# Optimization experiments

Hardware: AMD Instinct MI355X
Metric: run time of the kernel (lower is better)

## Reference

```python
import jax, jax.numpy as jnp
import numpy as np

B, S, D = 46, 50, 768
GAMA = 1.0 - 2.0 ** -5  # 1 - np.power(2.0, -5 - arange(0,1)) -> scalar 0.96875


def make_pe(n, d):
    # PositionalEncoding buffer pe[:n]; note original adds pe[:emb.size(0)],
    # i.e. the encoding is indexed by BATCH position (faithful to source).
    position = jnp.arange(n, dtype=jnp.float32)[:, None]
    div_term = jnp.exp(jnp.arange(0, d, 2, dtype=jnp.float32) * (-np.log(10000.0) / d))
    pe = jnp.zeros((n, d), dtype=jnp.float32)
    pe = pe.at[:, 0::2].set(jnp.sin(position * div_term))
    pe = pe.at[:, 1::2].set(jnp.cos(position * div_term))
    return pe[:, None, :]  # [n, 1, d] broadcasts over the seq dim


def setup_inputs() -> dict:
    key = jax.random.key(0)
    ks = jax.random.split(key, 6)
    w = lambda k, shape: jax.random.normal(k, shape, dtype=jnp.float32) * 0.02
    return {
        "text_embedding": jax.random.normal(ks[0], (B, S, D), dtype=jnp.float32),
        "embedding": jax.random.normal(ks[1], (B, S, D), dtype=jnp.float32),
        "Wq_w": w(ks[2], (D, D)), "Wq_b": jnp.zeros((D,), jnp.float32),
        "Wk_w": w(ks[3], (D, D)), "Wk_b": jnp.zeros((D,), jnp.float32),
        "Wv_w": w(ks[4], (D, D)), "Wv_b": jnp.zeros((D,), jnp.float32),
        "lin_w": w(ks[5], (S, D)), "lin_b": jnp.zeros((S,), jnp.float32),
    }


def reference(text_embedding, embedding, Wq_w, Wq_b, Wk_w, Wk_b, Wv_w, Wv_b, lin_w, lin_b):
    b = text_embedding.shape[0]
    pe = make_pe(b, D)  # [B,1,D]
    # dropout p=0.1 is identity in eval mode
    Q = text_embedding @ Wq_w.T + Wq_b + pe          # [B,S,D]
    K = embedding @ Wk_w.T + Wk_b + pe               # [B,S,D]
    V = embedding @ Wv_w.T + Wv_b                    # [B,S,D]
    # head_num == 1, so transpose_for_scores is a no-op view
    Q_trans = Q @ lin_w.T + lin_b                    # [B,S,S] (S == 50)
    scores = jnp.einsum('bqd,bkd->bqk', Q, K) * 8.0  # scaling *8 as in source
    probs = jax.nn.softmax(scores, axis=-1)
    ctx = jnp.einsum('bqk,bkd->bqd', probs, V)       # [B,S,D] context_layer

    # RetNet-like gamma-decay recurrence over the batch dim (host-sync loop in
    # the original, expressed here as an on-device lax.scan):
    #   s_i = Q_trans @ (gama * s_{i-1}) + ctx[i],  s_{-1} = 0
    def step(s, c_i):  # s: [B,S,D], c_i: [S,D]
        s_new = jnp.einsum('bij,bjd->bid', Q_trans, GAMA * s) + c_i[None]
        return s_new, s_new
    _, rec = jax.lax.scan(step, jnp.zeros_like(ctx), ctx)  # [B,B,S,D]
    return ctx, rec
```

## Files before the change

kernel.cpp:

```cpp
#include <hip/hip_runtime.h>
#include <math.h>

#define NB 46
#define NS 50
#define ND 768
#define GAMA 0.96875f
#define NM 2300

using bfrag  = __attribute__((ext_vector_type(8))) short;
using f32x16 = __attribute__((ext_vector_type(16))) float;

union FragU { unsigned u[4]; bfrag f; };

__device__ __forceinline__ void cvt_hilo(const float f[8], bfrag& fh, bfrag& fl)
{
    FragU uh, ul;
    #pragma unroll
    for (int t = 0; t < 4; t++) {
        const unsigned b0 = __float_as_uint(f[2 * t]);
        const unsigned b1 = __float_as_uint(f[2 * t + 1]);
        uh.u[t] = (b0 >> 16) | (b1 & 0xFFFF0000u);
        const float r0 = f[2 * t]     - __uint_as_float(b0 & 0xFFFF0000u);
        const float r1 = f[2 * t + 1] - __uint_as_float(b1 & 0xFFFF0000u);
        ul.u[t] = (__float_as_uint(r0) >> 16) | (__float_as_uint(r1) & 0xFFFF0000u);
    }
    fh = uh.f; fl = ul.f;
}

__global__ __launch_bounds__(256) void qkv_gemm(
    const float* __restrict__ text_emb, const float* __restrict__ emb,
    const float* __restrict__ Wq, const float* __restrict__ bq,
    const float* __restrict__ Wk, const float* __restrict__ bk,
    const float* __restrict__ Wv, const float* __restrict__ bv,
    float* __restrict__ Q, float* __restrict__ K, float* __restrict__ V)
{
    const int z = blockIdx.z;
    const float* X    = (z == 0) ? text_emb : emb;
    const float* W    = (z == 0) ? Wq : (z == 1) ? Wk : Wv;
    const float* bias = (z == 0) ? bq : (z == 1) ? bk : bv;
    float* out        = (z == 0) ? Q  : (z == 1) ? K  : V;

    __shared__ float Xs[32][68];
    __shared__ float Ws[32][68];

    const int tid = threadIdx.x;
    const int w   = tid >> 6;
    const int l   = tid & 63;
    const int c   = l & 31;
    const int h   = l >> 5;
    const int wm  = w >> 1, wn = w & 1;
    const int m0  = blockIdx.x * 64, n0 = blockIdx.y * 64;

    const int lrow = tid >> 2;
    const int lk   = (tid & 3) * 4;
    const int xm   = m0 + lrow;
    const float* __restrict__ Xrow = X + (size_t)(xm < NM ? xm : 0) * ND;
    const float* __restrict__ Wrow = W + (size_t)(n0 + lrow) * ND;

    f32x16 acc;
    #pragma unroll
    for (int g = 0; g < 16; g++) acc[g] = 0.f;

    for (int k0 = 0; k0 < ND; k0 += 32) {
        const float4 xv0 = *reinterpret_cast<const float4*>(&Xrow[k0 + lk]);
        const float4 xv1 = *reinterpret_cast<const float4*>(&Xrow[k0 + 16 + lk]);
        const float4 wv0 = *reinterpret_cast<const float4*>(&Wrow[k0 + lk]);
        const float4 wv1 = *reinterpret_cast<const float4*>(&Wrow[k0 + 16 + lk]);
        __syncthreads();
        Xs[lk + 0][lrow] = xv0.x; Xs[lk + 1][lrow] = xv0.y;
        Xs[lk + 2][lrow] = xv0.z; Xs[lk + 3][lrow] = xv0.w;
        Xs[16 + lk + 0][lrow] = xv1.x; Xs[16 + lk + 1][lrow] = xv1.y;
        Xs[16 + lk + 2][lrow] = xv1.z; Xs[16 + lk + 3][lrow] = xv1.w;
        Ws[lk + 0][lrow] = wv0.x; Ws[lk + 1][lrow] = wv0.y;
        Ws[lk + 2][lrow] = wv0.z; Ws[lk + 3][lrow] = wv0.w;
        Ws[16 + lk + 0][lrow] = wv1.x; Ws[16 + lk + 1][lrow] = wv1.y;
        Ws[16 + lk + 2][lrow] = wv1.z; Ws[16 + lk + 3][lrow] = wv1.w;
        __syncthreads();

        #pragma unroll
        for (int kt = 0; kt < 2; kt++) {
            float fx[8], fw[8];
            #pragma unroll
            for (int j = 0; j < 8; j++) {
                fx[j] = Xs[16 * kt + 8 * h + j][32 * wm + c];
                fw[j] = Ws[16 * kt + 8 * h + j][32 * wn + c];
            }
            bfrag Ah, Al, Bh, Bl;
            cvt_hilo(fx, Ah, Al);
            cvt_hilo(fw, Bh, Bl);
            acc = __builtin_amdgcn_mfma_f32_32x32x16_bf16(Ah, Bh, acc, 0, 0, 0);
            acc = __builtin_amdgcn_mfma_f32_32x32x16_bf16(Ah, Bl, acc, 0, 0, 0);
            acc = __builtin_amdgcn_mfma_f32_32x32x16_bf16(Al, Bh, acc, 0, 0, 0);
        }
    }

    const float C2 = -0.0239861701969175f;
    const int n = n0 + 32 * wn + c;
    #pragma unroll
    for (int g = 0; g < 16; g++) {
        const int rr = (g & 3) + 8 * (g >> 2) + 4 * h;
        const int m  = m0 + 32 * wm + rr;
        if (m >= NM) continue;
        float v = acc[g] + bias[n];
        if (z < 2) {
            const int bpos = m / NS;
            const float ang = (float)bpos * expf((float)(n >> 1) * C2);
            v += (n & 1) ? cosf(ang) : sinf(ang);
        }
        out[(size_t)m * ND + n] = v;
    }
}

__global__ __launch_bounds__(256, 1) void attn(
    const float* __restrict__ Q, const float* __restrict__ K,
    const float* __restrict__ V,
    const float* __restrict__ lin_w, const float* __restrict__ lin_b,
    float* __restrict__ Ag, float* __restrict__ ctx_out)
{
    const int b   = blockIdx.x;
    const int tid = threadIdx.x;
    const int w   = tid >> 6;
    const int l   = tid & 63;
    const int c   = l & 31;
    const int h   = l >> 5;

    __shared__ float Lsh[9 * 64 * 68];
    float* SP = Lsh;
    float* QP = Lsh + 4 * 64 * 68;
    float* Pf = Lsh + 8 * 64 * 68;

    const float* __restrict__ Qb = Q + (size_t)b * NS * ND;
    const float* __restrict__ Kb = K + (size_t)b * NS * ND;
    const float* __restrict__ Vb = V + (size_t)b * NS * ND;

    f32x16 accS[2][2], accQ[2][2];
    #pragma unroll
    for (int mt = 0; mt < 2; mt++)
        #pragma unroll
        for (int nt = 0; nt < 2; nt++)
            #pragma unroll
            for (int g = 0; g < 16; g++) { accS[mt][nt][g] = 0.f; accQ[mt][nt][g] = 0.f; }

    const int ks = w * 192;
    for (int kt = 0; kt < 12; ++kt) {
        const int ko = ks + kt * 16 + 8 * h;
        bfrag Qh[2], Ql[2], Kh[2], Kl[2], Wh[2], Wl[2];
        #pragma unroll
        for (int mt = 0; mt < 2; mt++) {
            const int row = 32 * mt + c;
            const int r = (row < NS) ? row : 0;
            float f[8];
            {
                const float4 a0 = *reinterpret_cast<const float4*>(&Qb[(size_t)r * ND + ko]);
                const float4 a1 = *reinterpret_cast<const float4*>(&Qb[(size_t)r * ND + ko + 4]);
                f[0]=a0.x; f[1]=a0.y; f[2]=a0.z; f[3]=a0.w; f[4]=a1.x; f[5]=a1.y; f[6]=a1.z; f[7]=a1.w;
            }
            cvt_hilo(f, Qh[mt], Ql[mt]);
            {
                const float4 a0 = *reinterpret_cast<const float4*>(&Kb[(size_t)r * ND + ko]);
                const float4 a1 = *reinterpret_cast<const float4*>(&Kb[(size_t)r * ND + ko + 4]);
                f[0]=a0.x; f[1]=a0.y; f[2]=a0.z; f[3]=a0.w; f[4]=a1.x; f[5]=a1.y; f[6]=a1.z; f[7]=a1.w;
            }
            cvt_hilo(f, Kh[mt], Kl[mt]);
            {
                const float4 a0 = *reinterpret_cast<const float4*>(&lin_w[(size_t)r * ND + ko]);
                const float4 a1 = *reinterpret_cast<const float4*>(&lin_w[(size_t)r * ND + ko + 4]);
                f[0]=a0.x; f[1]=a0.y; f[2]=a0.z; f[3]=a0.w; f[4]=a1.x; f[5]=a1.y; f[6]=a1.z; f[7]=a1.w;
            }
            cvt_hilo(f, Wh[mt], Wl[mt]);
        }
        #pragma unroll
        for (int mt = 0; mt < 2; mt++)
            #pragma unroll
            for (int nt = 0; nt < 2; nt++) {
                f32x16 a = accS[mt][nt];
                a = __builtin_amdgcn_mfma_f32_32x32x16_bf16(Qh[mt], Kh[nt], a, 0, 0, 0);
                a = __builtin_amdgcn_mfma_f32_32x32x16_bf16(Qh[mt], Kl[nt], a, 0, 0, 0);
                a = __builtin_amdgcn_mfma_f32_32x32x16_bf16(Ql[mt], Kh[nt], a, 0, 0, 0);
                accS[mt][nt] = a;
                f32x16 q = accQ[mt][nt];
                q = __builtin_amdgcn_mfma_f32_32x32x16_bf16(Qh[mt], Wh[nt], q, 0, 0, 0);
                q = __builtin_amdgcn_mfma_f32_32x32x16_bf16(Qh[mt], Wl[nt], q, 0, 0, 0);
                q = __builtin_amdgcn_mfma_f32_32x32x16_bf16(Ql[mt], Wh[nt], q, 0, 0, 0);
                accQ[mt][nt] = q;
            }
    }

    {
        float* SPw = SP + w * (64 * 68);
        float* QPw = QP + w * (64 * 68);
        #pragma unroll
        for (int mt = 0; mt < 2; mt++)
            #pragma unroll
            for (int nt = 0; nt < 2; nt++)
                #pragma unroll
                for (int g = 0; g < 16; g++) {
                    const int rg  = 32 * mt + (g & 3) + 8 * (g >> 2) + 4 * h;
                    const int col = 32 * nt + c;
                    SPw[rg * 68 + col] = accS[mt][nt][g];
                    QPw[rg * 68 + col] = accQ[mt][nt][g];
                }
    }
    __syncthreads();

    {
        const int r  = tid >> 2;
        const int cg = (tid & 3) * 16;
        #pragma unroll
        for (int q4 = 0; q4 < 4; ++q4) {
            const int off = r * 68 + cg + q4 * 4;
            float4 s0 = *reinterpret_cast<const float4*>(&SP[off]);
            float4 s1 = *reinterpret_cast<const float4*>(&SP[64 * 68 + off]);
            float4 s2 = *reinterpret_cast<const float4*>(&SP[2 * 64 * 68 + off]);
            float4 s3 = *reinterpret_cast<const float4*>(&SP[3 * 64 * 68 + off]);
            float4 r4;
            r4.x = 8.f * ((s0.x + s1.x) + (s2.x + s3.x));
            r4.y = 8.f * ((s0.y + s1.y) + (s2.y + s3.y));
            r4.z = 8.f * ((s0.z + s1.z) + (s2.z + s3.z));
            r4.w = 8.f * ((s0.w + s1.w) + (s2.w + s3.w));
            *reinterpret_cast<float4*>(&SP[off]) = r4;
            float4 t0 = *reinterpret_cast<const float4*>(&QP[off]);
            float4 t1 = *reinterpret_cast<const float4*>(&QP[64 * 68 + off]);
            float4 t2 = *reinterpret_cast<const float4*>(&QP[2 * 64 * 68 + off]);
            float4 t3 = *reinterpret_cast<const float4*>(&QP[3 * 64 * 68 + off]);
            float4 u4;
            u4.x = (t0.x + t1.x) + (t2.x + t3.x);
            u4.y = (t0.y + t1.y) + (t2.y + t3.y);
            u4.z = (t0.z + t1.z) + (t2.z + t3.z);
            u4.w = (t0.w + t1.w) + (t2.w + t3.w);
            *reinterpret_cast<float4*>(&QP[off]) = u4;
        }
    }
    __syncthreads();

    if (tid < NS) {
        const float* Sr = SP + tid * 68;
        float mx = -INFINITY;
        for (int c2 = 0; c2 < NS; ++c2) mx = fmaxf(mx, Sr[c2]);
        float sum = 0.f;
        for (int c2 = 0; c2 < NS; ++c2) {
            const float e = expf(Sr[c2] - mx);
            Pf[tid * 68 + c2] = e;
            sum += e;
        }
        const float inv = 1.f / sum;
        for (int c2 = 0; c2 < NS; ++c2) Pf[tid * 68 + c2] *= inv;
        for (int c2 = NS; c2 < 64; ++c2) Pf[tid * 68 + c2] = 0.f;
    }
    for (int e = tid; e < NS * NS; e += 256) {
        const int r = e / NS, cc = e - r * NS;
        Ag[b * (NS * NS) + e] = GAMA * (QP[r * 68 + cc] + lin_b[cc]);
    }
    __syncthreads();

    bfrag Ph[2][4], Pl[2][4];
    #pragma unroll
    for (int mt = 0; mt < 2; mt++)
        #pragma unroll
        for (int kt = 0; kt < 4; kt++) {
            float f[8];
            #pragma unroll
            for (int j = 0; j < 8; j++)
                f[j] = Pf[(32 * mt + c) * 68 + kt * 16 + 8 * h + j];
            cvt_hilo(f, Ph[mt][kt], Pl[mt][kt]);
        }

    for (int j3 = 0; j3 < 3; ++j3) {
        const int dbase = (w * 3 + j3) * 64;
        f32x16 accC[2][2];
        #pragma unroll
        for (int mt = 0; mt < 2; mt++)
            #pragma unroll
            for (int nt = 0; nt < 2; nt++)
                #pragma unroll
                for (int g = 0; g < 16; g++) accC[mt][nt][g] = 0.f;

        #pragma unroll
        for (int nt = 0; nt < 2; nt++) {
            const int d = dbase + 32 * nt + c;
            #pragma unroll
            for (int kt = 0; kt < 4; kt++) {
                float f[8];
                #pragma unroll
                for (int j = 0; j < 8; j++) {
                    const int k2 = kt * 16 + 8 * h + j;
                    f[j] = (k2 < NS) ? Vb[(size_t)k2 * ND + d] : 0.f;
                }
                bfrag Bh, Bl;
                cvt_hilo(f, Bh, Bl);
                #pragma unroll
                for (int mt = 0; mt < 2; mt++) {
                    f32x16 a = accC[mt][nt];
                    a = __builtin_amdgcn_mfma_f32_32x32x16_bf16(Ph[mt][kt], Bh, a, 0, 0, 0);
                    a = __builtin_amdgcn_mfma_f32_32x32x16_bf16(Ph[mt][kt], Bl, a, 0, 0, 0);
                    a = __builtin_amdgcn_mfma_f32_32x32x16_bf16(Pl[mt][kt], Bh, a, 0, 0, 0);
                    accC[mt][nt] = a;
                }
            }
        }
        #pragma unroll
        for (int mt = 0; mt < 2; mt++)
            #pragma unroll
            for (int nt = 0; nt < 2; nt++)
                #pragma unroll
                for (int g = 0; g < 16; g++) {
                    const int rg = 32 * mt + (g & 3) + 8 * (g >> 2) + 4 * h;
                    if (rg < NS)
                        ctx_out[((size_t)b * NS + rg) * ND + dbase + 32 * nt + c] = accC[mt][nt][g];
                }
    }
}

__device__ __forceinline__ void rec2_step(
    int i, int b, int d0, int c, int h, int wid, int srow, int scol,
    const bfrag (&Ah)[4], const bfrag (&Al)[4],
    float4 (&creg)[4],
    const float* SfR, float* SfW, float* Cx,
    const float* __restrict__ ctx, float* __restrict__ rec)
{
    #pragma unroll
    for (int it = 0; it < 4; ++it) {
        const int r = (4 * wid + it) * 8 + srow;
        if (r < NS)
            *reinterpret_cast<float4*>(&Cx[r * 32 + scol]) = creg[it];
    }
    if (i + 1 < NB) {
        const float* __restrict__ src = ctx + (size_t)(i + 1) * NS * ND + d0;
        #pragma unroll
        for (int it = 0; it < 4; ++it) {
            const int r = (4 * wid + it) * 8 + srow;
            if (r < NS)
                creg[it] = *reinterpret_cast<const float4*>(&src[(size_t)r * ND + scol]);
        }
    }
    f32x16 acc;
    #pragma unroll
    for (int g = 0; g < 16; g++) {
        const int rg = 32 * wid + (g & 3) + 8 * (g >> 2) + 4 * h;
        acc[g] = Cx[rg * 32 + c];
    }
    #pragma unroll
    for (int kt = 0; kt < 4; kt++) {
        float f[8];
        #pragma unroll
        for (int j = 0; j < 8; j++)
            f[j] = SfR[(16 * kt + 8 * h + j) * 32 + c];
        bfrag Bh, Bl;
        cvt_hilo(f, Bh, Bl);
        acc = __builtin_amdgcn_mfma_f32_32x32x16_bf16(Ah[kt], Bh, acc, 0, 0, 0);
        acc = __builtin_amdgcn_mfma_f32_32x32x16_bf16(Ah[kt], Bl, acc, 0, 0, 0);
        acc = __builtin_amdgcn_mfma_f32_32x32x16_bf16(Al[kt], Bh, acc, 0, 0, 0);
    }
    #pragma unroll
    for (int g = 0; g < 16; g++) {
        const int rg = 32 * wid + (g & 3) + 8 * (g >> 2) + 4 * h;
        SfW[rg * 32 + c] = acc[g];
    }
    float* __restrict__ reci = rec + (size_t)(i * NB + b) * NS * ND + d0;
    #pragma unroll
    for (int it = 0; it < 4; ++it) {
        const int r = (4 * wid + it) * 8 + srow;
        if (r < NS) {
            const float4 v = *reinterpret_cast<const float4*>(&SfW[r * 32 + scol]);
            *reinterpret_cast<float4*>(&reci[(size_t)r * ND + scol]) = v;
        }
    }
    asm volatile("s_waitcnt lgkmcnt(0)" ::: "memory");
    __builtin_amdgcn_s_barrier();
    asm volatile("" ::: "memory");
}

__global__ __launch_bounds__(128, 2) void recur(
    const float* __restrict__ Ag, const float* __restrict__ ctx,
    float* __restrict__ rec)
{
    const int blk   = blockIdx.x;
    const int b     = blk / 24;
    const int chunk = blk - b * 24;
    const int tid   = threadIdx.x;
    const int wid   = tid >> 6;
    const int l     = tid & 63;
    const int c     = l & 31;
    const int h     = l >> 5;
    const int d0    = chunk * 32;
    const int srow  = l >> 3;
    const int scol  = (l & 7) * 4;

    __shared__ float Sfa[64 * 32];
    __shared__ float Sfb[64 * 32];
    __shared__ float Cx [64 * 32];

    const float* __restrict__ Ab = Ag + b * (NS * NS);
    bfrag Ah[4], Al[4];
    {
        const int row = 32 * wid + c;
        const bool rok = row < NS;
        const float* __restrict__ Arow = Ab + row * NS;
        #pragma unroll
        for (int kt = 0; kt < 4; kt++) {
            FragU uh, ul;
            #pragma unroll
            for (int t = 0; t < 4; t++) {
                const int k0 = 16 * kt + 8 * h + 2 * t;
                const float e = (rok && k0     < NS) ? Arow[k0]     : 0.f;
                const float o = (rok && k0 + 1 < NS) ? Arow[k0 + 1] : 0.f;
                const unsigned ue = __float_as_uint(e), uo = __float_as_uint(o);
                uh.u[t] = (ue >> 16) | (uo & 0xFFFF0000u);
                const float re = e - __uint_as_float(ue & 0xFFFF0000u);
                const float ro = o - __uint_as_float(uo & 0xFFFF0000u);
                ul.u[t] = (__float_as_uint(re) >> 16) | (__float_as_uint(ro) & 0xFFFF0000u);
            }
            Ah[kt] = uh.f; Al[kt] = ul.f;
        }
    }

    for (int idx = tid; idx < 14 * 32; idx += 128) {
        const int rr = 50 + (idx >> 5), cc = idx & 31;
        Cx [rr * 32 + cc] = 0.f;
        Sfa[rr * 32 + cc] = 0.f;
    }

    float4 creg[4];
    #pragma unroll
    for (int it = 0; it < 4; ++it) creg[it] = make_float4(0.f, 0.f, 0.f, 0.f);
    {
        const float* __restrict__ src = ctx + d0;
        float4 c0[4];
        #pragma unroll
        for (int it = 0; it < 4; ++it) {
            c0[it] = make_float4(0.f, 0.f, 0.f, 0.f);
            const int r = (4 * wid + it) * 8 + srow;
            if (r < NS)
                c0[it] = *reinterpret_cast<const float4*>(&src[(size_t)r * ND + scol]);
        }
        const float* __restrict__ s1 = ctx + (size_t)NS * ND + d0;
        #pragma unroll
        for (int it = 0; it < 4; ++it) {
            const int r = (4 * wid + it) * 8 + srow;
            if (r < NS)
                creg[it] = *reinterpret_cast<const float4*>(&s1[(size_t)r * ND + scol]);
        }
        float* __restrict__ r0 = rec + (size_t)b * NS * ND + d0;
        #pragma unroll
        for (int it = 0; it < 4; ++it) {
            const int r = (4 * wid + it) * 8 + srow;
            if (r < NS) {
                *reinterpret_cast<float4*>(&Sfa[r * 32 + scol]) = c0[it];
                *reinterpret_cast<float4*>(&r0[(size_t)r * ND + scol]) = c0[it];
            }
        }
    }
    asm volatile("s_waitcnt lgkmcnt(0)" ::: "memory");
    __builtin_amdgcn_s_barrier();
    asm volatile("" ::: "memory");

    int i = 1;
    for (; i + 1 < NB; i += 2) {
        rec2_step(i,     b, d0, c, h, wid, srow, scol, Ah, Al, creg, Sfa, Sfb, Cx, ctx, rec);
        rec2_step(i + 1, b, d0, c, h, wid, srow, scol, Ah, Al, creg, Sfb, Sfa, Cx, ctx, rec);
    }
    if (i < NB)
        rec2_step(i, b, d0, c, h, wid, srow, scol, Ah, Al, creg, Sfa, Sfb, Cx, ctx, rec);
}

extern "C" void kernel_launch(void* const* d_in, const int* in_sizes, int n_in,
                              void* d_out, int out_size, void* d_ws, size_t ws_size,
                              hipStream_t stream) {
    const float* text_emb = (const float*)d_in[0];
    const float* emb      = (const float*)d_in[1];
    const float* Wq = (const float*)d_in[2]; const float* bq = (const float*)d_in[3];
    const float* Wk = (const float*)d_in[4]; const float* bk = (const float*)d_in[5];
    const float* Wv = (const float*)d_in[6]; const float* bv = (const float*)d_in[7];
    const float* lw = (const float*)d_in[8]; const float* lb = (const float*)d_in[9];

    float* out = (float*)d_out;
    float* ctx = out;
    float* rec = out + NB * NS * ND;

    float* ws = (float*)d_ws;
    float* Q  = ws;
    float* K  = Q + NB * NS * ND;
    float* V  = K + NB * NS * ND;
    float* Ag = V + NB * NS * ND;

    qkv_gemm<<<dim3(36, 12, 3), 256, 0, stream>>>(text_emb, emb, Wq, bq, Wk, bk, Wv, bv, Q, K, V);
    attn<<<dim3(NB), 256, 0, stream>>>(Q, K, V, lw, lb, Ag, ctx);
    recur<<<dim3(1104), 128, 0, stream>>>(Ag, ctx, rec);
}
```

Before: 206.0 us.

## Restructure recurrence kernel to single-wave blocks with 16x16 MFMA tiles

The recurrence kernel now runs one 64-thread wave per block over a 16-column slice (2208 blocks), using 16x16x32 bf16 MFMA with four M-tiles instead of two waves with 32x32x16 tiles. Because a single wave owns the whole 64-row state tile, the per-step workgroup barrier and double-buffered shared state are removed and a single in-place buffer is used. This aims to remove the barrier latency on the serial 45-step chain and raise parallelism, at the cost of more blocks, narrower 64-byte global row segments, and more MFMA issues per step per wave.

```diff
diff --git a/kernel.cpp b/kernel.cpp
--- a/kernel.cpp
+++ b/kernel.cpp
@@ -9,6 +9,7 @@
 
 using bfrag  = __attribute__((ext_vector_type(8))) short;
 using f32x16 = __attribute__((ext_vector_type(16))) float;
+using f32x4  = __attribute__((ext_vector_type(4)))  float;
 
 union FragU { unsigned u[4]; bfrag f; };
 
@@ -311,97 +312,36 @@
     }
 }
 
-__device__ __forceinline__ void rec2_step(
-    int i, int b, int d0, int c, int h, int wid, int srow, int scol,
-    const bfrag (&Ah)[4], const bfrag (&Al)[4],
-    float4 (&creg)[4],
-    const float* SfR, float* SfW, float* Cx,
-    const float* __restrict__ ctx, float* __restrict__ rec)
-{
-    #pragma unroll
-    for (int it = 0; it < 4; ++it) {
-        const int r = (4 * wid + it) * 8 + srow;
-        if (r < NS)
-            *reinterpret_cast<float4*>(&Cx[r * 32 + scol]) = creg[it];
-    }
-    if (i + 1 < NB) {
-        const float* __restrict__ src = ctx + (size_t)(i + 1) * NS * ND + d0;
-        #pragma unroll
-        for (int it = 0; it < 4; ++it) {
-            const int r = (4 * wid + it) * 8 + srow;
-            if (r < NS)
-                creg[it] = *reinterpret_cast<const float4*>(&src[(size_t)r * ND + scol]);
-        }
-    }
-    f32x16 acc;
-    #pragma unroll
-    for (int g = 0; g < 16; g++) {
-        const int rg = 32 * wid + (g & 3) + 8 * (g >> 2) + 4 * h;
-        acc[g] = Cx[rg * 32 + c];
-    }
-    #pragma unroll
-    for (int kt = 0; kt < 4; kt++) {
-        float f[8];
-        #pragma unroll
-        for (int j = 0; j < 8; j++)
-            f[j] = SfR[(16 * kt + 8 * h + j) * 32 + c];
-        bfrag Bh, Bl;
-        cvt_hilo(f, Bh, Bl);
-        acc = __builtin_amdgcn_mfma_f32_32x32x16_bf16(Ah[kt], Bh, acc, 0, 0, 0);
-        acc = __builtin_amdgcn_mfma_f32_32x32x16_bf16(Ah[kt], Bl, acc, 0, 0, 0);
-        acc = __builtin_amdgcn_mfma_f32_32x32x16_bf16(Al[kt], Bh, acc, 0, 0, 0);
-    }
-    #pragma unroll
-    for (int g = 0; g < 16; g++) {
-        const int rg = 32 * wid + (g & 3) + 8 * (g >> 2) + 4 * h;
-        SfW[rg * 32 + c] = acc[g];
-    }
-    float* __restrict__ reci = rec + (size_t)(i * NB + b) * NS * ND + d0;
-    #pragma unroll
-    for (int it = 0; it < 4; ++it) {
-        const int r = (4 * wid + it) * 8 + srow;
-        if (r < NS) {
-            const float4 v = *reinterpret_cast<const float4*>(&SfW[r * 32 + scol]);
-            *reinterpret_cast<float4*>(&reci[(size_t)r * ND + scol]) = v;
-        }
-    }
-    asm volatile("s_waitcnt lgkmcnt(0)" ::: "memory");
-    __builtin_amdgcn_s_barrier();
-    asm volatile("" ::: "memory");
-}
-
-__global__ __launch_bounds__(128, 2) void recur(
+__global__ __launch_bounds__(64, 1) void recur(
     const float* __restrict__ Ag, const float* __restrict__ ctx,
     float* __restrict__ rec)
 {
     const int blk   = blockIdx.x;
-    const int b     = blk / 24;
-    const int chunk = blk - b * 24;
-    const int tid   = threadIdx.x;
-    const int wid   = tid >> 6;
-    const int l     = tid & 63;
-    const int c     = l & 31;
-    const int h     = l >> 5;
-    const int d0    = chunk * 32;
-    const int srow  = l >> 3;
-    const int scol  = (l & 7) * 4;
-
-    __shared__ float Sfa[64 * 32];
-    __shared__ float Sfb[64 * 32];
-    __shared__ float Cx [64 * 32];
+    const int b     = blk / 48;
+    const int chunk = blk - b * 48;
+    const int l     = threadIdx.x;
+    const int c16   = l & 15;
+    const int q4    = l >> 4;
+    const int d0    = chunk * 16;
+    const int srow  = l >> 2;
+    const int scol  = (l & 3) * 4;
+
+    __shared__ float Sf[64 * 16];
+    __shared__ float Cx[64 * 16];
 
     const float* __restrict__ Ab = Ag + b * (NS * NS);
-    bfrag Ah[4], Al[4];
-    {
-        const int row = 32 * wid + c;
+    bfrag Ah[4][2], Al[4][2];
+    #pragma unroll
+    for (int mt = 0; mt < 4; mt++) {
+        const int row = 16 * mt + c16;
         const bool rok = row < NS;
         const float* __restrict__ Arow = Ab + row * NS;
         #pragma unroll
-        for (int kt = 0; kt < 4; kt++) {
+        for (int kt = 0; kt < 2; kt++) {
             FragU uh, ul;
             #pragma unroll
             for (int t = 0; t < 4; t++) {
-                const int k0 = 16 * kt + 8 * h + 2 * t;
+                const int k0 = 32 * kt + 8 * q4 + 2 * t;
                 const float e = (rok && k0     < NS) ? Arow[k0]     : 0.f;
                 const float o = (rok && k0 + 1 < NS) ? Arow[k0 + 1] : 0.f;
                 const unsigned ue = __float_as_uint(e), uo = __float_as_uint(o);
@@ -410,14 +350,14 @@
                 const float ro = o - __uint_as_float(uo & 0xFFFF0000u);
                 ul.u[t] = (__float_as_uint(re) >> 16) | (__float_as_uint(ro) & 0xFFFF0000u);
             }
-            Ah[kt] = uh.f; Al[kt] = ul.f;
-        }
-    }
-
-    for (int idx = tid; idx < 14 * 32; idx += 128) {
-        const int rr = 50 + (idx >> 5), cc = idx & 31;
-        Cx [rr * 32 + cc] = 0.f;
-        Sfa[rr * 32 + cc] = 0.f;
+            Ah[mt][kt] = uh.f; Al[mt][kt] = ul.f;
+        }
+    }
+
+    {
+        const float4 z = make_float4(0.f, 0.f, 0.f, 0.f);
+        *reinterpret_cast<float4*>(&Cx[(48 + srow) * 16 + scol]) = z;
+        *reinterpret_cast<float4*>(&Sf[(48 + srow) * 16 + scol]) = z;
     }
 
     float4 creg[4];
@@ -429,38 +369,92 @@
         #pragma unroll
         for (int it = 0; it < 4; ++it) {
             c0[it] = make_float4(0.f, 0.f, 0.f, 0.f);
-            const int r = (4 * wid + it) * 8 + srow;
+            const int r = it * 16 + srow;
             if (r < NS)
                 c0[it] = *reinterpret_cast<const float4*>(&src[(size_t)r * ND + scol]);
         }
         const float* __restrict__ s1 = ctx + (size_t)NS * ND + d0;
         #pragma unroll
         for (int it = 0; it < 4; ++it) {
-            const int r = (4 * wid + it) * 8 + srow;
+            const int r = it * 16 + srow;
             if (r < NS)
                 creg[it] = *reinterpret_cast<const float4*>(&s1[(size_t)r * ND + scol]);
         }
         float* __restrict__ r0 = rec + (size_t)b * NS * ND + d0;
         #pragma unroll
         for (int it = 0; it < 4; ++it) {
-            const int r = (4 * wid + it) * 8 + srow;
+            const int r = it * 16 + srow;
             if (r < NS) {
-                *reinterpret_cast<float4*>(&Sfa[r * 32 + scol]) = c0[it];
+                *reinterpret_cast<float4*>(&Sf[r * 16 + scol]) = c0[it];
                 *reinterpret_cast<float4*>(&r0[(size_t)r * ND + scol]) = c0[it];
             }
         }
     }
-    asm volatile("s_waitcnt lgkmcnt(0)" ::: "memory");
-    __builtin_amdgcn_s_barrier();
-    asm volatile("" ::: "memory");
-
-    int i = 1;
-    for (; i + 1 < NB; i += 2) {
-        rec2_step(i,     b, d0, c, h, wid, srow, scol, Ah, Al, creg, Sfa, Sfb, Cx, ctx, rec);
-        rec2_step(i + 1, b, d0, c, h, wid, srow, scol, Ah, Al, creg, Sfb, Sfa, Cx, ctx, rec);
-    }
-    if (i < NB)
-        rec2_step(i, b, d0, c, h, wid, srow, scol, Ah, Al, creg, Sfa, Sfb, Cx, ctx, rec);
+
+    for (int i = 1; i < NB; ++i) {
+        #pragma unroll
+        for (int it = 0; it < 4; ++it) {
+            const int r = it * 16 + srow;
+            if (r < NS)
+                *reinterpret_cast<float4*>(&Cx[r * 16 + scol]) = creg[it];
+        }
+        if (i + 1 < NB) {
+            const float* __restrict__ src = ctx + (size_t)(i + 1) * NS * ND + d0;
+            #pragma unroll
+            for (int it = 0; it < 4; ++it) {
+                const int r = it * 16 + srow;
+                if (r < NS)
+                    creg[it] = *reinterpret_cast<const float4*>(&src[(size_t)r * ND + scol]);
+            }
+        }
+        f32x4 acc[4];
+        #pragma unroll
+        for (int mt = 0; mt < 4; mt++)
+            #pragma unroll
+            for (int g = 0; g < 4; g++) {
+                const int rg = 16 * mt + 4 * q4 + g;
+                acc[mt][g] = Cx[rg * 16 + c16];
+            }
+        bfrag Bh[2], Bl[2];
+        #pragma unroll
+        for (int kt = 0; kt < 2; kt++) {
+            float f[8];
+            #pragma unroll
+            for (int j = 0; j < 8; j++)
+                f[j] = Sf[(32 * kt + 8 * q4 + j) * 16 + c16];
+            cvt_hilo(f, Bh[kt], Bl[kt]);
+        }
+        #pragma unroll
+        for (int mt = 0; mt < 4; mt++) {
+            f32x4 a = acc[mt];
+            #pragma unroll
+            for (int kt = 0; kt < 2; kt++)
+                a = __builtin_amdgcn_mfma_f32_16x16x32_bf16(Ah[mt][kt], Bh[kt], a, 0, 0, 0);
+            #pragma unroll
+            for (int kt = 0; kt < 2; kt++)
+                a = __builtin_amdgcn_mfma_f32_16x16x32_bf16(Ah[mt][kt], Bl[kt], a, 0, 0, 0);
+            #pragma unroll
+            for (int kt = 0; kt < 2; kt++)
+                a = __builtin_amdgcn_mfma_f32_16x16x32_bf16(Al[mt][kt], Bh[kt], a, 0, 0, 0);
+            acc[mt] = a;
+        }
+        #pragma unroll
+        for (int mt = 0; mt < 4; mt++)
+            #pragma unroll
+            for (int g = 0; g < 4; g++) {
+                const int rg = 16 * mt + 4 * q4 + g;
+                Sf[rg * 16 + c16] = acc[mt][g];
+            }
+        float* __restrict__ reci = rec + (size_t)(i * NB + b) * NS * ND + d0;
+        #pragma unroll
+        for (int it = 0; it < 4; ++it) {
+            const int r = it * 16 + srow;
+            if (r < NS) {
+                const float4 v = *reinterpret_cast<const float4*>(&Sf[r * 16 + scol]);
+                *reinterpret_cast<float4*>(&reci[(size_t)r * ND + scol]) = v;
+            }
+        }
+    }
 }
 
 extern "C" void kernel_launch(void* const* d_in, const int* in_sizes, int n_in,
@@ -485,5 +479,5 @@
 
     qkv_gemm<<<dim3(36, 12, 3), 256, 0, stream>>>(text_emb, emb, Wq, bq, Wk, bk, Wv, bv, Q, K, V);
     attn<<<dim3(NB), 256, 0, stream>>>(Q, K, V, lw, lb, Ag, ctx);
-    recur<<<dim3(1104), 128, 0, stream>>>(Ag, ctx, rec);
+    recur<<<dim3(2208), 64, 0, stream>>>(Ag, ctx, rec);
 }
```

Result: faster. 198.0 us (-3.9%).
